# Kernel tuning notes

Hardware: AMD Instinct MI355X
Metric: run time of the kernel (lower is better)

## Reference

```python
import jax, jax.numpy as jnp
import numpy as np

N_NODES = 50000
N_EDGES = 600000
D_IN = 128
HID = 128
N_SAGE = 2          # num_layers - 1
N_GRAPHS = 512
BN_EPS = 1e-5


def setup_inputs() -> dict:
    key = jax.random.key(0)
    ks = jax.random.split(key, 12)
    s = 1.0 / np.sqrt(HID)
    x = jax.random.normal(ks[0], (N_NODES, D_IN), dtype=jnp.float32)
    edge_index = jax.random.randint(ks[1], (2, N_EDGES), 0, N_NODES, dtype=jnp.int32)
    batch = jnp.sort(jax.random.randint(ks[2], (N_NODES,), 0, N_GRAPHS, dtype=jnp.int32))
    # GIN MLP: Linear(D_IN,HID) -> ReLU -> Linear(HID,HID)
    gin_w1 = jax.random.normal(ks[3], (D_IN, HID), dtype=jnp.float32) * s
    gin_b1 = jnp.zeros((HID,), jnp.float32)
    gin_w2 = jax.random.normal(ks[4], (HID, HID), dtype=jnp.float32) * s
    gin_b2 = jnp.zeros((HID,), jnp.float32)
    # SAGEConv layers: lin_l (neighbors, with bias), lin_r (root, no bias)
    sage_wl = jax.random.normal(ks[5], (N_SAGE, HID, HID), dtype=jnp.float32) * s
    sage_bl = jnp.zeros((N_SAGE, HID), jnp.float32)
    sage_wr = jax.random.normal(ks[6], (N_SAGE, HID, HID), dtype=jnp.float32) * s
    # BatchNorm per layer (3 layers)
    bn_gamma = jnp.ones((1 + N_SAGE, HID), jnp.float32)
    bn_beta = jnp.zeros((1 + N_SAGE, HID), jnp.float32)
    return {"x": x, "edge_index": edge_index, "batch": batch,
            "gin_w1": gin_w1, "gin_b1": gin_b1, "gin_w2": gin_w2, "gin_b2": gin_b2,
            "sage_wl": sage_wl, "sage_bl": sage_bl, "sage_wr": sage_wr,
            "bn_gamma": bn_gamma, "bn_beta": bn_beta}


def _batchnorm(h, gamma, beta):
    # training-mode BN over the node dimension (biased variance, as torch)
    mu = jnp.mean(h, axis=0)
    var = jnp.var(h, axis=0)
    return gamma * (h - mu) * jax.lax.rsqrt(var + BN_EPS) + beta


def reference(x, edge_index, batch, gin_w1, gin_b1, gin_w2, gin_b2,
              sage_wl, sage_bl, sage_wr, bn_gamma, bn_beta):
    n = x.shape[0]
    src, dst = edge_index[0], edge_index[1]

    # ---- Layer 0: GINConv (eps=0): mlp(x + sum_{j->i} x_j) ----
    agg = jax.ops.segment_sum(x[src], dst, num_segments=n)  # [N, D_IN]
    h = x + agg
    h = jax.nn.relu(h @ gin_w1 + gin_b1) @ gin_w2 + gin_b2
    h = jax.nn.relu(_batchnorm(h, bn_gamma[0], bn_beta[0]))
    # dropout is identity (eval mode)

    # degree for mean aggregation (shared across SAGE layers)
    deg = jax.ops.segment_sum(jnp.ones((src.shape[0],), h.dtype), dst, num_segments=n)
    inv_deg = (1.0 / jnp.maximum(deg, 1.0))[:, None]  # [N,1]

    # ---- SAGE layers: lin_l(mean_{j->i} h_j) + lin_r(h_i) ----
    for l in range(N_SAGE):
        neigh = jax.ops.segment_sum(h[src], dst, num_segments=n) * inv_deg
        h = neigh @ sage_wl[l] + sage_bl[l] + h @ sage_wr[l]
        h = jax.nn.relu(_batchnorm(h, bn_gamma[l + 1], bn_beta[l + 1]))

    # ---- global mean pool over batch ids ----
    sums = jax.ops.segment_sum(h, batch, num_segments=N_GRAPHS)  # [G, HID]
    counts = jax.ops.segment_sum(jnp.ones((n,), h.dtype), batch, num_segments=N_GRAPHS)
    return sums / jnp.maximum(counts, 1.0)[:, None]
```

## Files before the change

kernel.cpp:

```cpp
#include <hip/hip_runtime.h>

#define N_NODES 50000
#define N_EDGES 600000
#define HID 128
#define N_GRAPHS 512
#define BN_EPS 1e-5f
#define INV_N (1.0f / 50000.0f)
#define NGROUPS 3125
#define FUSED_GRID 1024
#define IDXCAP 2048

typedef __attribute__((ext_vector_type(8))) short bf16x8;
typedef __attribute__((ext_vector_type(4))) float f32x4;

__device__ __forceinline__ unsigned short f2b(float f) {
    unsigned u = __float_as_uint(f);
    return (unsigned short)((u + 0x7FFFu + ((u >> 16) & 1u)) >> 16);
}
__device__ __forceinline__ float b2f(unsigned short h) {
    return __uint_as_float(((unsigned)h) << 16);
}

__device__ __forceinline__ float stats_sum(const float* __restrict__ s, int idx) {
    float v = 0.f;
#pragma unroll
    for (int r = 0; r < 8; r++) v += s[r * 256 + idx];
    return v;
}

#define CONVX_BLOCKS 6250
#define WCONV_BLOCKS 384
#define DEG_BLOCKS   2344
__global__ __launch_bounds__(256) void prep_kernel(
    const float* __restrict__ x, const float* __restrict__ gw1, const float* __restrict__ gw2,
    const float* __restrict__ swl, const float* __restrict__ swr, const int* __restrict__ dst,
    unsigned short* __restrict__ x16, unsigned short* __restrict__ wt, int* __restrict__ deg)
{
    int b = blockIdx.x;
    int t = threadIdx.x;
    if (b < CONVX_BLOCKS) {
        int gid = b * 256 + t;
        int i = gid >> 5, l = gid & 31;
        if (i >= N_NODES) return;
        int c0 = l * 4;
        float4 v = *(const float4*)(x + (size_t)i * 128 + c0);
        ushort4 o;
        o.x = f2b(v.x); o.y = f2b(v.y); o.z = f2b(v.z); o.w = f2b(v.w);
        *(ushort4*)(x16 + (size_t)i * 128 + c0) = o;
    } else if (b < CONVX_BLOCKS + WCONV_BLOCKS) {
        int gid = (b - CONVX_BLOCKS) * 256 + t;
        int m = gid >> 14;
        int e = gid & 16383;
        int k = e >> 7;
        int n = e & 127;
        const float* src = (m == 0) ? gw1 : (m == 1) ? gw2 : (m == 2) ? swl
                         : (m == 3) ? swr : (m == 4) ? (swl + 16384) : (swr + 16384);
        wt[m * 16384 + n * 128 + k] = f2b(src[k * 128 + n]);
    } else {
        int e = (b - CONVX_BLOCKS - WCONV_BLOCKS) * 256 + t;
        if (e < N_EDGES) atomicAdd(&deg[dst[e]], 1);
    }
}

#define ALLOC_BLOCKS 196
__global__ __launch_bounds__(256) void alloc_kernel(int* __restrict__ cursor,
                                                    int* __restrict__ row_beg,
                                                    float* __restrict__ inv_deg,
                                                    int* __restrict__ total,
                                                    const int* __restrict__ batch,
                                                    int* __restrict__ gstart) {
    if (blockIdx.x >= ALLOC_BLOCKS) {
        int g = (blockIdx.x - ALLOC_BLOCKS) * 256 + threadIdx.x;
        if (g > N_GRAPHS) return;
        int lo = 0, hi = N_NODES;
        while (lo < hi) {
            int mid = (lo + hi) >> 1;
            if (batch[mid] < g) lo = mid + 1; else hi = mid;
        }
        gstart[g] = lo;
        return;
    }
    __shared__ int tmp[256];
    __shared__ int base;
    int i = blockIdx.x * 256 + threadIdx.x;
    int d = (i < N_NODES) ? cursor[i] : 0;
    tmp[threadIdx.x] = d;
    __syncthreads();
#pragma unroll
    for (int off = 1; off < 256; off <<= 1) {
        int v = (threadIdx.x >= off) ? tmp[threadIdx.x - off] : 0;
        __syncthreads();
        tmp[threadIdx.x] += v;
        __syncthreads();
    }
    if (threadIdx.x == 255) base = atomicAdd(total, tmp[255]);
    __syncthreads();
    if (i < N_NODES) {
        int b = base + tmp[threadIdx.x] - d;
        row_beg[i] = b;
        cursor[i] = b;
        inv_deg[i] = 1.0f / fmaxf((float)d, 1.0f);
    }
}

__global__ void csr_fill_kernel(const int* __restrict__ src, const int* __restrict__ dst,
                                int* __restrict__ cursor, unsigned short* __restrict__ csr_src, int nE) {
    int e = blockIdx.x * blockDim.x + threadIdx.x;
    if (e < nE) {
        int pos = atomicAdd(&cursor[dst[e]], 1);
        csr_src[pos] = (unsigned short)src[e];
    }
}

template<bool AFF>
__device__ __forceinline__ void gather_row(
    const unsigned short* __restrict__ feat,
    const unsigned short* __restrict__ csr_src,
    const unsigned short* __restrict__ idxbuf,
    bool lds_ok, int ebeg, int beg, int deg, int c0,
    const float (&cc)[8], const float (&ss)[8], float (&a)[8])
{
#pragma unroll
    for (int j = 0; j < 8; j++) a[j] = 0.f;
    if (lds_ok) {
        const int off = beg - ebeg;
        int e = 0;
        for (; e + 7 < deg; e += 8) {
            int s[8];
#pragma unroll
            for (int u = 0; u < 8; u++) s[u] = idxbuf[off + e + u];
            bf16x8 v[8];
#pragma unroll
            for (int u = 0; u < 8; u++)
                v[u] = *(const bf16x8*)(feat + (size_t)s[u] * 128 + c0);
#pragma unroll
            for (int u = 0; u < 8; u++)
#pragma unroll
                for (int j = 0; j < 8; j++) {
                    float tv = b2f((unsigned short)v[u][j]);
                    if (AFF) tv = fmaxf(tv * cc[j] + ss[j], 0.f);
                    a[j] += tv;
                }
        }
        for (; e + 3 < deg; e += 4) {
            int s[4];
#pragma unroll
            for (int u = 0; u < 4; u++) s[u] = idxbuf[off + e + u];
            bf16x8 v[4];
#pragma unroll
            for (int u = 0; u < 4; u++)
                v[u] = *(const bf16x8*)(feat + (size_t)s[u] * 128 + c0);
#pragma unroll
            for (int u = 0; u < 4; u++)
#pragma unroll
                for (int j = 0; j < 8; j++) {
                    float tv = b2f((unsigned short)v[u][j]);
                    if (AFF) tv = fmaxf(tv * cc[j] + ss[j], 0.f);
                    a[j] += tv;
                }
        }
        for (; e < deg; e++) {
            int s0 = idxbuf[off + e];
            bf16x8 v0 = *(const bf16x8*)(feat + (size_t)s0 * 128 + c0);
#pragma unroll
            for (int j = 0; j < 8; j++) {
                float tv = b2f((unsigned short)v0[j]);
                if (AFF) tv = fmaxf(tv * cc[j] + ss[j], 0.f);
                a[j] += tv;
            }
        }
    } else {
        for (int e = beg; e < beg + deg; e++) {
            int s0 = csr_src[e];
            bf16x8 v0 = *(const bf16x8*)(feat + (size_t)s0 * 128 + c0);
#pragma unroll
            for (int j = 0; j < 8; j++) {
                float tv = b2f((unsigned short)v0[j]);
                if (AFF) tv = fmaxf(tv * cc[j] + ss[j], 0.f);
                a[j] += tv;
            }
        }
    }
}

__global__ __launch_bounds__(256, 2) void fused_gin_kernel(
    const unsigned short* __restrict__ X,
    const int* __restrict__ row_beg, const int* __restrict__ row_end,
    const unsigned short* __restrict__ csr_src,
    const unsigned short* __restrict__ W1t, const unsigned short* __restrict__ W2t,
    const float* __restrict__ b1, const float* __restrict__ b2,
    float* __restrict__ stats_out, unsigned short* __restrict__ Hout, int ngroups)
{
    __shared__ unsigned short idxbuf[IDXCAP];
    __shared__ unsigned short aT[16][136];
    __shared__ unsigned short t1[16][136];
    __shared__ float red[128];

    const int t = threadIdx.x;
    const int wave = t >> 6;
    const int lane = t & 63;
    const int m16 = lane & 15;
    const int quad = lane >> 4;
    const int k0 = quad * 8;
    const int colbase = wave * 32;
    const int nslot = t >> 4;
    const int c0 = (t & 15) * 8;

    bf16x8 w1f[2][4], w2f[2][4];
#pragma unroll
    for (int ct = 0; ct < 2; ct++) {
        int col = colbase + ct * 16 + m16;
#pragma unroll
        for (int kc = 0; kc < 4; kc++) {
            w1f[ct][kc] = *(const bf16x8*)(W1t + (size_t)col * 128 + kc * 32 + k0);
            w2f[ct][kc] = *(const bf16x8*)(W2t + (size_t)col * 128 + kc * 32 + k0);
        }
    }
    f32x4 bs1[2], bs2[2];
#pragma unroll
    for (int ct = 0; ct < 2; ct++) {
        bs1[ct] = *(const f32x4*)(b1 + colbase + ct * 16 + quad * 4);
        bs2[ct] = *(const f32x4*)(b2 + colbase + ct * 16 + quad * 4);
    }

    float psum[2][4], psq[2][4];
#pragma unroll
    for (int ct = 0; ct < 2; ct++)
#pragma unroll
        for (int r = 0; r < 4; r++) { psum[ct][r] = 0.f; psq[ct][r] = 0.f; }

    float dcc[8], dss[8];
#pragma unroll
    for (int j = 0; j < 8; j++) { dcc[j] = 0.f; dss[j] = 0.f; }

    for (int g = blockIdx.x; g < ngroups; g += gridDim.x) {
        const int node0 = g * 16;
        const int node = node0 + nslot;
        const int ebeg = row_beg[node0];
        const int ecnt = row_end[node0 + 15] - ebeg;
        const bool lds_ok = (ecnt <= IDXCAP);
        if (lds_ok)
            for (int i = t; i < ecnt; i += 256) idxbuf[i] = csr_src[ebeg + i];
        bf16x8 vself = *(const bf16x8*)(X + (size_t)node * 128 + c0);
        const int beg = row_beg[node];
        const int deg = row_end[node] - beg;
        __syncthreads();

        float a[8];
        gather_row<false>(X, csr_src, idxbuf, lds_ok, ebeg, beg, deg, c0, dcc, dss, a);

        bf16x8 arow;
#pragma unroll
        for (int j = 0; j < 8; j++)
            arow[j] = (short)f2b(a[j] + b2f((unsigned short)vself[j]));
        *(bf16x8*)&aT[nslot][c0] = arow;
        __syncthreads();

        bf16x8 af[4];
#pragma unroll
        for (int kc = 0; kc < 4; kc++)
            af[kc] = *(const bf16x8*)&aT[m16][kc * 32 + k0];
        f32x4 acc[2];
        acc[0] = (f32x4){0.f, 0.f, 0.f, 0.f};
        acc[1] = (f32x4){0.f, 0.f, 0.f, 0.f};
#pragma unroll
        for (int kc = 0; kc < 4; kc++)
#pragma unroll
            for (int ct = 0; ct < 2; ct++)
                acc[ct] = __builtin_amdgcn_mfma_f32_16x16x32_bf16(w1f[ct][kc], af[kc], acc[ct], 0, 0, 0);
#pragma unroll
        for (int ct = 0; ct < 2; ct++) {
            f32x4 v = acc[ct] + bs1[ct];
            ushort4 o;
            o.x = f2b(fmaxf(v[0], 0.f));
            o.y = f2b(fmaxf(v[1], 0.f));
            o.z = f2b(fmaxf(v[2], 0.f));
            o.w = f2b(fmaxf(v[3], 0.f));
            *(ushort4*)&t1[m16][colbase + ct * 16 + quad * 4] = o;
        }
        __syncthreads();

        bf16x8 tf[4];
#pragma unroll
        for (int kc = 0; kc < 4; kc++)
            tf[kc] = *(const bf16x8*)&t1[m16][kc * 32 + k0];
        f32x4 acc2[2];
        acc2[0] = (f32x4){0.f, 0.f, 0.f, 0.f};
        acc2[1] = (f32x4){0.f, 0.f, 0.f, 0.f};
#pragma unroll
        for (int kc = 0; kc < 4; kc++)
#pragma unroll
            for (int ct = 0; ct < 2; ct++)
                acc2[ct] = __builtin_amdgcn_mfma_f32_16x16x32_bf16(w2f[ct][kc], tf[kc], acc2[ct], 0, 0, 0);

        const int orow = node0 + m16;
#pragma unroll
        for (int ct = 0; ct < 2; ct++) {
            f32x4 v = acc2[ct] + bs2[ct];
            int col = colbase + ct * 16 + quad * 4;
#pragma unroll
            for (int r = 0; r < 4; r++) { psum[ct][r] += v[r]; psq[ct][r] += v[r] * v[r]; }
            ushort4 o;
            o.x = f2b(v[0]); o.y = f2b(v[1]); o.z = f2b(v[2]); o.w = f2b(v[3]);
            *(ushort4*)(Hout + (size_t)orow * 128 + col) = o;
        }
    }

#pragma unroll
    for (int ct = 0; ct < 2; ct++)
#pragma unroll
        for (int r = 0; r < 4; r++)
#pragma unroll
            for (int mask = 1; mask <= 8; mask <<= 1) {
                psum[ct][r] += __shfl_xor(psum[ct][r], mask, 64);
                psq[ct][r]  += __shfl_xor(psq[ct][r], mask, 64);
            }
    __syncthreads();
    if (m16 == 0)
#pragma unroll
        for (int ct = 0; ct < 2; ct++)
#pragma unroll
            for (int r = 0; r < 4; r++)
                red[colbase + ct * 16 + quad * 4 + r] = psum[ct][r];
    __syncthreads();
    if (t < 128) atomicAdd(&stats_out[(blockIdx.x & 7) * 256 + t], red[t]);
    __syncthreads();
    if (m16 == 0)
#pragma unroll
        for (int ct = 0; ct < 2; ct++)
#pragma unroll
            for (int r = 0; r < 4; r++)
                red[colbase + ct * 16 + quad * 4 + r] = psq[ct][r];
    __syncthreads();
    if (t < 128) atomicAdd(&stats_out[(blockIdx.x & 7) * 256 + 128 + t], red[t]);
}

__global__ __launch_bounds__(256, 2) void fused_sage_kernel(
    const unsigned short* __restrict__ Hin,
    const int* __restrict__ row_beg, const int* __restrict__ row_end,
    const unsigned short* __restrict__ csr_src,
    const float* __restrict__ stats_in, const float* __restrict__ gamma,
    const float* __restrict__ beta, const float* __restrict__ inv_deg,
    const unsigned short* __restrict__ Wlt, const unsigned short* __restrict__ Wrt,
    const float* __restrict__ bias, float* __restrict__ stats_out,
    unsigned short* __restrict__ Hout, int ngroups)
{
    __shared__ unsigned short idxbuf[IDXCAP];
    __shared__ unsigned short aT[16][136];
    __shared__ unsigned short hT[16][136];
    __shared__ float red[128];

    const int t = threadIdx.x;
    const int wave = t >> 6;
    const int lane = t & 63;
    const int m16 = lane & 15;
    const int quad = lane >> 4;
    const int k0 = quad * 8;
    const int colbase = wave * 32;
    const int nslot = t >> 4;
    const int c0 = (t & 15) * 8;

    float cc[8], ss[8];
#pragma unroll
    for (int j = 0; j < 8; j++) {
        int col = c0 + j;
        float mu = stats_sum(stats_in, col) * INV_N;
        float var = stats_sum(stats_in, 128 + col) * INV_N - mu * mu;
        float rs = rsqrtf(var + BN_EPS);
        float c = gamma[col] * rs;
        cc[j] = c;
        ss[j] = beta[col] - mu * c;
    }

    bf16x8 wl[2][4], wr[2][4];
#pragma unroll
    for (int ct = 0; ct < 2; ct++) {
        int col = colbase + ct * 16 + m16;
#pragma unroll
        for (int kc = 0; kc < 4; kc++) {
            wl[ct][kc] = *(const bf16x8*)(Wlt + (size_t)col * 128 + kc * 32 + k0);
            wr[ct][kc] = *(const bf16x8*)(Wrt + (size_t)col * 128 + kc * 32 + k0);
        }
    }
    f32x4 bs[2];
#pragma unroll
    for (int ct = 0; ct < 2; ct++)
        bs[ct] = *(const f32x4*)(bias + colbase + ct * 16 + quad * 4);

    float psum[2][4], psq[2][4];
#pragma unroll
    for (int ct = 0; ct < 2; ct++)
#pragma unroll
        for (int r = 0; r < 4; r++) { psum[ct][r] = 0.f; psq[ct][r] = 0.f; }

    for (int g = blockIdx.x; g < ngroups; g += gridDim.x) {
        const int node0 = g * 16;
        const int node = node0 + nslot;
        const int ebeg = row_beg[node0];
        const int ecnt = row_end[node0 + 15] - ebeg;
        const bool lds_ok = (ecnt <= IDXCAP);
        if (lds_ok)
            for (int i = t; i < ecnt; i += 256) idxbuf[i] = csr_src[ebeg + i];
        bf16x8 vself = *(const bf16x8*)(Hin + (size_t)node * 128 + c0);
        const float sc = inv_deg[node];
        const int beg = row_beg[node];
        const int deg = row_end[node] - beg;
        __syncthreads();

        float a[8];
        gather_row<true>(Hin, csr_src, idxbuf, lds_ok, ebeg, beg, deg, c0, cc, ss, a);

        bf16x8 arow, hrow;
#pragma unroll
        for (int j = 0; j < 8; j++) {
            arow[j] = (short)f2b(a[j] * sc);
            hrow[j] = (short)f2b(fmaxf(b2f((unsigned short)vself[j]) * cc[j] + ss[j], 0.f));
        }
        *(bf16x8*)&aT[nslot][c0] = arow;
        *(bf16x8*)&hT[nslot][c0] = hrow;
        __syncthreads();

        bf16x8 a1[4], a2[4];
#pragma unroll
        for (int kc = 0; kc < 4; kc++) {
            a1[kc] = *(const bf16x8*)&aT[m16][kc * 32 + k0];
            a2[kc] = *(const bf16x8*)&hT[m16][kc * 32 + k0];
        }
        f32x4 acc[2];
        acc[0] = (f32x4){0.f, 0.f, 0.f, 0.f};
        acc[1] = (f32x4){0.f, 0.f, 0.f, 0.f};
#pragma unroll
        for (int kc = 0; kc < 4; kc++)
#pragma unroll
            for (int ct = 0; ct < 2; ct++) {
                acc[ct] = __builtin_amdgcn_mfma_f32_16x16x32_bf16(wl[ct][kc], a1[kc], acc[ct], 0, 0, 0);
                acc[ct] = __builtin_amdgcn_mfma_f32_16x16x32_bf16(wr[ct][kc], a2[kc], acc[ct], 0, 0, 0);
            }

        const int orow = node0 + m16;
#pragma unroll
        for (int ct = 0; ct < 2; ct++) {
            f32x4 v = acc[ct] + bs[ct];
            int col = colbase + ct * 16 + quad * 4;
#pragma unroll
            for (int r = 0; r < 4; r++) { psum[ct][r] += v[r]; psq[ct][r] += v[r] * v[r]; }
            ushort4 o;
            o.x = f2b(v[0]); o.y = f2b(v[1]); o.z = f2b(v[2]); o.w = f2b(v[3]);
            *(ushort4*)(Hout + (size_t)orow * 128 + col) = o;
        }
    }

#pragma unroll
    for (int ct = 0; ct < 2; ct++)
#pragma unroll
        for (int r = 0; r < 4; r++)
#pragma unroll
            for (int mask = 1; mask <= 8; mask <<= 1) {
                psum[ct][r] += __shfl_xor(psum[ct][r], mask, 64);
                psq[ct][r]  += __shfl_xor(psq[ct][r], mask, 64);
            }
    __syncthreads();
    if (m16 == 0)
#pragma unroll
        for (int ct = 0; ct < 2; ct++)
#pragma unroll
            for (int r = 0; r < 4; r++)
                red[colbase + ct * 16 + quad * 4 + r] = psum[ct][r];
    __syncthreads();
    if (t < 128) atomicAdd(&stats_out[(blockIdx.x & 7) * 256 + t], red[t]);
    __syncthreads();
    if (m16 == 0)
#pragma unroll
        for (int ct = 0; ct < 2; ct++)
#pragma unroll
            for (int r = 0; r < 4; r++)
                red[colbase + ct * 16 + quad * 4 + r] = psq[ct][r];
    __syncthreads();
    if (t < 128) atomicAdd(&stats_out[(blockIdx.x & 7) * 256 + 128 + t], red[t]);
}

__global__ __launch_bounds__(128) void pool_mean_kernel(const unsigned short* __restrict__ h,
                                                        const int* __restrict__ gstart,
                                                        const float* __restrict__ stats,
                                                        const float* __restrict__ gamma,
                                                        const float* __restrict__ beta,
                                                        float* __restrict__ out) {
    __shared__ float red[8][128];
    int g = blockIdx.x;
    int t = threadIdx.x;
    int lane = t & 15, grp = t >> 4;
    int c0 = lane * 8;
    float c[8], b[8];
#pragma unroll
    for (int j = 0; j < 8; j++) {
        int col = c0 + j;
        float mu = stats_sum(stats, col) * INV_N;
        float var = stats_sum(stats, 128 + col) * INV_N - mu * mu;
        float rs = rsqrtf(var + BN_EPS);
        c[j] = gamma[col] * rs;
        b[j] = beta[col] - mu * c[j];
    }
    int beg = gstart[g];
    int end = gstart[g + 1];
    float s[8];
#pragma unroll
    for (int j = 0; j < 8; j++) s[j] = 0.f;
    for (int i = beg + grp; i < end; i += 8) {
        bf16x8 v = *(const bf16x8*)(h + (size_t)i * 128 + c0);
#pragma unroll
        for (int j = 0; j < 8; j++)
            s[j] += fmaxf(b2f((unsigned short)v[j]) * c[j] + b[j], 0.f);
    }
#pragma unroll
    for (int j = 0; j < 8; j++) red[grp][c0 + j] = s[j];
    __syncthreads();
    if (t < 16) {
        float cnt = fmaxf((float)(end - beg), 1.0f);
        int cc0 = t * 8;
#pragma unroll
        for (int j = 0; j < 8; j++) {
            float tot = 0.f;
#pragma unroll
            for (int r = 0; r < 8; r++) tot += red[r][cc0 + j];
            out[(size_t)g * 128 + cc0 + j] = tot / cnt;
        }
    }
}

extern "C" void kernel_launch(void* const* d_in, const int* in_sizes, int n_in,
                              void* d_out, int out_size, void* d_ws, size_t ws_size,
                              hipStream_t stream) {
    const float* x    = (const float*)d_in[0];
    const int*   ei   = (const int*)d_in[1];
    const int*   src  = ei;
    const int*   dst  = ei + N_EDGES;
    const int*   batch = (const int*)d_in[2];
    const float* gw1  = (const float*)d_in[3];
    const float* gb1  = (const float*)d_in[4];
    const float* gw2  = (const float*)d_in[5];
    const float* gb2  = (const float*)d_in[6];
    const float* swl  = (const float*)d_in[7];
    const float* sbl  = (const float*)d_in[8];
    const float* swr  = (const float*)d_in[9];
    const float* bng  = (const float*)d_in[10];
    const float* bnb  = (const float*)d_in[11];
    float* out = (float*)d_out;

    float* ws = (float*)d_ws;
    unsigned short* x16    = (unsigned short*)(ws + 0);
    unsigned short* h_a    = (unsigned short*)(ws + 3200000);
    unsigned short* h_b    = (unsigned short*)(ws + 6400000);
    unsigned short* wt     = (unsigned short*)(ws + 12800000);
    float*          inv_deg= ws + 12850000;
    int*            row_beg= (int*)(ws + 12900000);
    int*            cursor = (int*)(ws + 12950000);
    int*            total  = cursor + 50000;
    float*          stats  = (float*)(cursor + 50001);
    unsigned short* csr_src= (unsigned short*)(ws + 13100000);
    int*            gstart = (int*)(ws + 13700000);

    hipMemsetAsync(cursor, 0, (50001 + 3 * 8 * 256) * sizeof(int), stream);

    prep_kernel<<<CONVX_BLOCKS + WCONV_BLOCKS + DEG_BLOCKS, 256, 0, stream>>>(
        x, gw1, gw2, swl, swr, dst, x16, wt, cursor);

    alloc_kernel<<<ALLOC_BLOCKS + 3, 256, 0, stream>>>(cursor, row_beg, inv_deg, total, batch, gstart);
    csr_fill_kernel<<<(N_EDGES + 255) / 256, 256, 0, stream>>>(src, dst, cursor, csr_src, N_EDGES);

    fused_gin_kernel<<<FUSED_GRID, 256, 0, stream>>>(
        x16, row_beg, cursor, csr_src, wt + 0 * 16384, wt + 1 * 16384,
        gb1, gb2, stats + 0 * 2048, h_a, NGROUPS);

    fused_sage_kernel<<<FUSED_GRID, 256, 0, stream>>>(
        h_a, row_beg, cursor, csr_src, stats + 0 * 2048, bng + 0 * HID, bnb + 0 * HID,
        inv_deg, wt + 2 * 16384, wt + 3 * 16384, sbl + 0 * HID, stats + 1 * 2048, h_b, NGROUPS);

    fused_sage_kernel<<<FUSED_GRID, 256, 0, stream>>>(
        h_b, row_beg, cursor, csr_src, stats + 1 * 2048, bng + 1 * HID, bnb + 1 * HID,
        inv_deg, wt + 4 * 16384, wt + 5 * 16384, sbl + 1 * HID, stats + 2 * 2048, h_a, NGROUPS);

    pool_mean_kernel<<<N_GRAPHS, 128, 0, stream>>>(
        h_a, gstart, stats + 2 * 2048, bng + 2 * HID, bnb + 2 * HID, out);
}
```

Before: 313.7 us.

## Split BN+ReLU into separate pass and launch one block per node group

Moves the BatchNorm affine and ReLU out of the SAGE gather loop into a standalone elementwise finish kernel, so neighbor gathers read already-activated features instead of applying the affine to every gathered element. The persistent grid-stride loop is replaced with one block per 16-node group. Weight fragments are loaded per half-tile to cut register pressure, which allows launch bounds of 6 blocks per SM, and the LDS index buffer is halved. This trades an extra read and write of the hidden matrix, plus two extra launches, for cheaper gathers and higher occupancy, and it reloads the weights in every block.

Result: slower. 320.5 us (+2.2%).

```diff
diff --git a/kernel.cpp b/kernel.cpp
--- a/kernel.cpp
+++ b/kernel.cpp
@@ -7,8 +7,7 @@
 #define BN_EPS 1e-5f
 #define INV_N (1.0f / 50000.0f)
 #define NGROUPS 3125
-#define FUSED_GRID 1024
-#define IDXCAP 2048
+#define IDXCAP 1024
 
 typedef __attribute__((ext_vector_type(8))) short bf16x8;
 typedef __attribute__((ext_vector_type(4))) float f32x4;
@@ -112,13 +111,11 @@
     }
 }
 
-template<bool AFF>
-__device__ __forceinline__ void gather_row(
+__device__ __forceinline__ void gather8(
     const unsigned short* __restrict__ feat,
     const unsigned short* __restrict__ csr_src,
     const unsigned short* __restrict__ idxbuf,
-    bool lds_ok, int ebeg, int beg, int deg, int c0,
-    const float (&cc)[8], const float (&ss)[8], float (&a)[8])
+    bool lds_ok, int ebeg, int beg, int deg, int c0, float (&a)[8])
 {
 #pragma unroll
     for (int j = 0; j < 8; j++) a[j] = 0.f;
@@ -136,11 +133,8 @@
 #pragma unroll
             for (int u = 0; u < 8; u++)
 #pragma unroll
-                for (int j = 0; j < 8; j++) {
-                    float tv = b2f((unsigned short)v[u][j]);
-                    if (AFF) tv = fmaxf(tv * cc[j] + ss[j], 0.f);
-                    a[j] += tv;
-                }
+                for (int j = 0; j < 8; j++)
+                    a[j] += b2f((unsigned short)v[u][j]);
         }
         for (; e + 3 < deg; e += 4) {
             int s[4];
@@ -153,43 +147,62 @@
 #pragma unroll
             for (int u = 0; u < 4; u++)
 #pragma unroll
-                for (int j = 0; j < 8; j++) {
-                    float tv = b2f((unsigned short)v[u][j]);
-                    if (AFF) tv = fmaxf(tv * cc[j] + ss[j], 0.f);
-                    a[j] += tv;
-                }
+                for (int j = 0; j < 8; j++)
+                    a[j] += b2f((unsigned short)v[u][j]);
         }
         for (; e < deg; e++) {
             int s0 = idxbuf[off + e];
             bf16x8 v0 = *(const bf16x8*)(feat + (size_t)s0 * 128 + c0);
 #pragma unroll
-            for (int j = 0; j < 8; j++) {
-                float tv = b2f((unsigned short)v0[j]);
-                if (AFF) tv = fmaxf(tv * cc[j] + ss[j], 0.f);
-                a[j] += tv;
-            }
+            for (int j = 0; j < 8; j++)
+                a[j] += b2f((unsigned short)v0[j]);
         }
     } else {
         for (int e = beg; e < beg + deg; e++) {
             int s0 = csr_src[e];
             bf16x8 v0 = *(const bf16x8*)(feat + (size_t)s0 * 128 + c0);
 #pragma unroll
-            for (int j = 0; j < 8; j++) {
-                float tv = b2f((unsigned short)v0[j]);
-                if (AFF) tv = fmaxf(tv * cc[j] + ss[j], 0.f);
-                a[j] += tv;
-            }
-        }
-    }
-}
-
-__global__ __launch_bounds__(256, 2) void fused_gin_kernel(
+            for (int j = 0; j < 8; j++)
+                a[j] += b2f((unsigned short)v0[j]);
+        }
+    }
+}
+
+__global__ __launch_bounds__(256) void finish_kernel(
+    const unsigned short* __restrict__ Hpre, const float* __restrict__ stats,
+    const float* __restrict__ gamma, const float* __restrict__ beta,
+    unsigned short* __restrict__ Hact)
+{
+    __shared__ float cs[2][128];
+    int t = threadIdx.x;
+    if (t < 128) {
+        float mu = stats_sum(stats, t) * INV_N;
+        float var = stats_sum(stats, 128 + t) * INV_N - mu * mu;
+        float rs = rsqrtf(var + BN_EPS);
+        float c = gamma[t] * rs;
+        cs[0][t] = c;
+        cs[1][t] = beta[t] - mu * c;
+    }
+    __syncthreads();
+    int gid = blockIdx.x * 256 + t;
+    int node = gid >> 4, l = gid & 15;
+    if (node >= N_NODES) return;
+    int c0 = l * 8;
+    bf16x8 v = *(const bf16x8*)(Hpre + (size_t)node * 128 + c0);
+    bf16x8 o;
+#pragma unroll
+    for (int j = 0; j < 8; j++)
+        o[j] = (short)f2b(fmaxf(b2f((unsigned short)v[j]) * cs[0][c0 + j] + cs[1][c0 + j], 0.f));
+    *(bf16x8*)(Hact + (size_t)node * 128 + c0) = o;
+}
+
+__global__ __launch_bounds__(256, 6) void fused_gin_kernel(
     const unsigned short* __restrict__ X,
     const int* __restrict__ row_beg, const int* __restrict__ row_end,
     const unsigned short* __restrict__ csr_src,
     const unsigned short* __restrict__ W1t, const unsigned short* __restrict__ W2t,
     const float* __restrict__ b1, const float* __restrict__ b2,
-    float* __restrict__ stats_out, unsigned short* __restrict__ Hout, int ngroups)
+    float* __restrict__ stats_out, unsigned short* __restrict__ Hout)
 {
     __shared__ unsigned short idxbuf[IDXCAP];
     __shared__ unsigned short aT[16][136];
@@ -202,148 +215,115 @@
     const int m16 = lane & 15;
     const int quad = lane >> 4;
     const int k0 = quad * 8;
-    const int colbase = wave * 32;
     const int nslot = t >> 4;
     const int c0 = (t & 15) * 8;
 
-    bf16x8 w1f[2][4], w2f[2][4];
-#pragma unroll
-    for (int ct = 0; ct < 2; ct++) {
-        int col = colbase + ct * 16 + m16;
+    const int g = blockIdx.x;
+    const int node0 = g * 16;
+    const int node = node0 + nslot;
+    const int ebeg = row_beg[node0];
+    const int ecnt = row_end[node0 + 15] - ebeg;
+    const bool lds_ok = (ecnt <= IDXCAP);
+    if (lds_ok)
+        for (int i = t; i < ecnt; i += 256) idxbuf[i] = csr_src[ebeg + i];
+    bf16x8 vself = *(const bf16x8*)(X + (size_t)node * 128 + c0);
+    const int beg = row_beg[node];
+    const int deg = row_end[node] - beg;
+    __syncthreads();
+
+    float a[8];
+    gather8(X, csr_src, idxbuf, lds_ok, ebeg, beg, deg, c0, a);
+
+    bf16x8 arow;
+#pragma unroll
+    for (int j = 0; j < 8; j++)
+        arow[j] = (short)f2b(a[j] + b2f((unsigned short)vself[j]));
+    *(bf16x8*)&aT[nslot][c0] = arow;
+    __syncthreads();
+
+#pragma unroll
+    for (int p = 0; p < 2; p++) {
+        const int cb = p * 64 + wave * 16;
+        bf16x8 wf[4];
+#pragma unroll
+        for (int kc = 0; kc < 4; kc++)
+            wf[kc] = *(const bf16x8*)(W1t + (size_t)(cb + m16) * 128 + kc * 32 + k0);
+        f32x4 bsv = *(const f32x4*)(b1 + cb + quad * 4);
+        f32x4 acc = (f32x4){0.f, 0.f, 0.f, 0.f};
 #pragma unroll
         for (int kc = 0; kc < 4; kc++) {
-            w1f[ct][kc] = *(const bf16x8*)(W1t + (size_t)col * 128 + kc * 32 + k0);
-            w2f[ct][kc] = *(const bf16x8*)(W2t + (size_t)col * 128 + kc * 32 + k0);
-        }
-    }
-    f32x4 bs1[2], bs2[2];
-#pragma unroll
-    for (int ct = 0; ct < 2; ct++) {
-        bs1[ct] = *(const f32x4*)(b1 + colbase + ct * 16 + quad * 4);
-        bs2[ct] = *(const f32x4*)(b2 + colbase + ct * 16 + quad * 4);
-    }
+            bf16x8 af = *(const bf16x8*)&aT[m16][kc * 32 + k0];
+            acc = __builtin_amdgcn_mfma_f32_16x16x32_bf16(wf[kc], af, acc, 0, 0, 0);
+        }
+        f32x4 v = acc + bsv;
+        ushort4 o;
+        o.x = f2b(fmaxf(v[0], 0.f));
+        o.y = f2b(fmaxf(v[1], 0.f));
+        o.z = f2b(fmaxf(v[2], 0.f));
+        o.w = f2b(fmaxf(v[3], 0.f));
+        *(ushort4*)&t1[m16][cb + quad * 4] = o;
+    }
+    __syncthreads();
 
     float psum[2][4], psq[2][4];
 #pragma unroll
-    for (int ct = 0; ct < 2; ct++)
-#pragma unroll
-        for (int r = 0; r < 4; r++) { psum[ct][r] = 0.f; psq[ct][r] = 0.f; }
-
-    float dcc[8], dss[8];
-#pragma unroll
-    for (int j = 0; j < 8; j++) { dcc[j] = 0.f; dss[j] = 0.f; }
-
-    for (int g = blockIdx.x; g < ngroups; g += gridDim.x) {
-        const int node0 = g * 16;
-        const int node = node0 + nslot;
-        const int ebeg = row_beg[node0];
-        const int ecnt = row_end[node0 + 15] - ebeg;
-        const bool lds_ok = (ecnt <= IDXCAP);
-        if (lds_ok)
-            for (int i = t; i < ecnt; i += 256) idxbuf[i] = csr_src[ebeg + i];
-        bf16x8 vself = *(const bf16x8*)(X + (size_t)node * 128 + c0);
-        const int beg = row_beg[node];
-        const int deg = row_end[node] - beg;
-        __syncthreads();
-
-        float a[8];
-        gather_row<false>(X, csr_src, idxbuf, lds_ok, ebeg, beg, deg, c0, dcc, dss, a);
-
-        bf16x8 arow;
-#pragma unroll
-        for (int j = 0; j < 8; j++)
-            arow[j] = (short)f2b(a[j] + b2f((unsigned short)vself[j]));
-        *(bf16x8*)&aT[nslot][c0] = arow;
-        __syncthreads();
-
-        bf16x8 af[4];
+    for (int p = 0; p < 2; p++) {
+        const int cb = p * 64 + wave * 16;
+        bf16x8 wf[4];
 #pragma unroll
         for (int kc = 0; kc < 4; kc++)
-            af[kc] = *(const bf16x8*)&aT[m16][kc * 32 + k0];
-        f32x4 acc[2];
-        acc[0] = (f32x4){0.f, 0.f, 0.f, 0.f};
-        acc[1] = (f32x4){0.f, 0.f, 0.f, 0.f};
-#pragma unroll
-        for (int kc = 0; kc < 4; kc++)
-#pragma unroll
-            for (int ct = 0; ct < 2; ct++)
-                acc[ct] = __builtin_amdgcn_mfma_f32_16x16x32_bf16(w1f[ct][kc], af[kc], acc[ct], 0, 0, 0);
-#pragma unroll
-        for (int ct = 0; ct < 2; ct++) {
-            f32x4 v = acc[ct] + bs1[ct];
-            ushort4 o;
-            o.x = f2b(fmaxf(v[0], 0.f));
-            o.y = f2b(fmaxf(v[1], 0.f));
-            o.z = f2b(fmaxf(v[2], 0.f));
-            o.w = f2b(fmaxf(v[3], 0.f));
-            *(ushort4*)&t1[m16][colbase + ct * 16 + quad * 4] = o;
-        }
-        __syncthreads();
-
-        bf16x8 tf[4];
-#pragma unroll
-        for (int kc = 0; kc < 4; kc++)
-            tf[kc] = *(const bf16x8*)&t1[m16][kc * 32 + k0];
-        f32x4 acc2[2];
-        acc2[0] = (f32x4){0.f, 0.f, 0.f, 0.f};
-        acc2[1] = (f32x4){0.f, 0.f, 0.f, 0.f};
-#pragma unroll
-        for (int kc = 0; kc < 4; kc++)
-#pragma unroll
-            for (int ct = 0; ct < 2; ct++)
-                acc2[ct] = __builtin_amdgcn_mfma_f32_16x16x32_bf16(w2f[ct][kc], tf[kc], acc2[ct], 0, 0, 0);
-
-        const int orow = node0 + m16;
-#pragma unroll
-        for (int ct = 0; ct < 2; ct++) {
-            f32x4 v = acc2[ct] + bs2[ct];
-            int col = colbase + ct * 16 + quad * 4;
-#pragma unroll
-            for (int r = 0; r < 4; r++) { psum[ct][r] += v[r]; psq[ct][r] += v[r] * v[r]; }
-            ushort4 o;
-            o.x = f2b(v[0]); o.y = f2b(v[1]); o.z = f2b(v[2]); o.w = f2b(v[3]);
-            *(ushort4*)(Hout + (size_t)orow * 128 + col) = o;
-        }
-    }
-
-#pragma unroll
-    for (int ct = 0; ct < 2; ct++)
+            wf[kc] = *(const bf16x8*)(W2t + (size_t)(cb + m16) * 128 + kc * 32 + k0);
+        f32x4 bsv = *(const f32x4*)(b2 + cb + quad * 4);
+        f32x4 acc = (f32x4){0.f, 0.f, 0.f, 0.f};
+#pragma unroll
+        for (int kc = 0; kc < 4; kc++) {
+            bf16x8 tf = *(const bf16x8*)&t1[m16][kc * 32 + k0];
+            acc = __builtin_amdgcn_mfma_f32_16x16x32_bf16(wf[kc], tf, acc, 0, 0, 0);
+        }
+        f32x4 v = acc + bsv;
+#pragma unroll
+        for (int r = 0; r < 4; r++) { psum[p][r] = v[r]; psq[p][r] = v[r] * v[r]; }
+        ushort4 o;
+        o.x = f2b(v[0]); o.y = f2b(v[1]); o.z = f2b(v[2]); o.w = f2b(v[3]);
+        *(ushort4*)(Hout + (size_t)(node0 + m16) * 128 + cb + quad * 4) = o;
+    }
+
+#pragma unroll
+    for (int p = 0; p < 2; p++)
 #pragma unroll
         for (int r = 0; r < 4; r++)
 #pragma unroll
             for (int mask = 1; mask <= 8; mask <<= 1) {
-                psum[ct][r] += __shfl_xor(psum[ct][r], mask, 64);
-                psq[ct][r]  += __shfl_xor(psq[ct][r], mask, 64);
+                psum[p][r] += __shfl_xor(psum[p][r], mask, 64);
+                psq[p][r]  += __shfl_xor(psq[p][r], mask, 64);
             }
-    __syncthreads();
     if (m16 == 0)
 #pragma unroll
-        for (int ct = 0; ct < 2; ct++)
+        for (int p = 0; p < 2; p++)
 #pragma unroll
             for (int r = 0; r < 4; r++)
-                red[colbase + ct * 16 + quad * 4 + r] = psum[ct][r];
-    __syncthreads();
-    if (t < 128) atomicAdd(&stats_out[(blockIdx.x & 7) * 256 + t], red[t]);
+                red[p * 64 + wave * 16 + quad * 4 + r] = psum[p][r];
+    __syncthreads();
+    if (t < 128) atomicAdd(&stats_out[(g & 7) * 256 + t], red[t]);
     __syncthreads();
     if (m16 == 0)
 #pragma unroll
-        for (int ct = 0; ct < 2; ct++)
+        for (int p = 0; p < 2; p++)
 #pragma unroll
             for (int r = 0; r < 4; r++)
-                red[colbase + ct * 16 + quad * 4 + r] = psq[ct][r];
-    __syncthreads();
-    if (t < 128) atomicAdd(&stats_out[(blockIdx.x & 7) * 256 + 128 + t], red[t]);
-}
-
-__global__ __launch_bounds__(256, 2) void fused_sage_kernel(
+                red[p * 64 + wave * 16 + quad * 4 + r] = psq[p][r];
+    __syncthreads();
+    if (t < 128) atomicAdd(&stats_out[(g & 7) * 256 + 128 + t], red[t]);
+}
+
+__global__ __launch_bounds__(256, 6) void fused_sage_kernel(
     const unsigned short* __restrict__ Hin,
     const int* __restrict__ row_beg, const int* __restrict__ row_end,
     const unsigned short* __restrict__ csr_src,
-    const float* __restrict__ stats_in, const float* __restrict__ gamma,
-    const float* __restrict__ beta, const float* __restrict__ inv_deg,
+    const float* __restrict__ inv_deg,
     const unsigned short* __restrict__ Wlt, const unsigned short* __restrict__ Wrt,
     const float* __restrict__ bias, float* __restrict__ stats_out,
-    unsigned short* __restrict__ Hout, int ngroups)
+    unsigned short* __restrict__ Hout)
 {
     __shared__ unsigned short idxbuf[IDXCAP];
     __shared__ unsigned short aT[16][136];
@@ -356,127 +336,87 @@
     const int m16 = lane & 15;
     const int quad = lane >> 4;
     const int k0 = quad * 8;
-    const int colbase = wave * 32;
     const int nslot = t >> 4;
     const int c0 = (t & 15) * 8;
 
-    float cc[8], ss[8];
-#pragma unroll
-    for (int j = 0; j < 8; j++) {
-        int col = c0 + j;
-        float mu = stats_sum(stats_in, col) * INV_N;
-        float var = stats_sum(stats_in, 128 + col) * INV_N - mu * mu;
-        float rs = rsqrtf(var + BN_EPS);
-        float c = gamma[col] * rs;
-        cc[j] = c;
-        ss[j] = beta[col] - mu * c;
-    }
-
-    bf16x8 wl[2][4], wr[2][4];
-#pragma unroll
-    for (int ct = 0; ct < 2; ct++) {
-        int col = colbase + ct * 16 + m16;
+    const int g = blockIdx.x;
+    const int node0 = g * 16;
+    const int node = node0 + nslot;
+    const int ebeg = row_beg[node0];
+    const int ecnt = row_end[node0 + 15] - ebeg;
+    const bool lds_ok = (ecnt <= IDXCAP);
+    if (lds_ok)
+        for (int i = t; i < ecnt; i += 256) idxbuf[i] = csr_src[ebeg + i];
+    bf16x8 vself = *(const bf16x8*)(Hin + (size_t)node * 128 + c0);
+    const float sc = inv_deg[node];
+    const int beg = row_beg[node];
+    const int deg = row_end[node] - beg;
+    __syncthreads();
+
+    float a[8];
+    gather8(Hin, csr_src, idxbuf, lds_ok, ebeg, beg, deg, c0, a);
+
+    bf16x8 arow;
+#pragma unroll
+    for (int j = 0; j < 8; j++)
+        arow[j] = (short)f2b(a[j] * sc);
+    *(bf16x8*)&aT[nslot][c0] = arow;
+    *(bf16x8*)&hT[nslot][c0] = vself;
+    __syncthreads();
+
+    float psum[2][4], psq[2][4];
+#pragma unroll
+    for (int p = 0; p < 2; p++) {
+        const int cb = p * 64 + wave * 16;
+        bf16x8 wl[4], wr[4];
 #pragma unroll
         for (int kc = 0; kc < 4; kc++) {
-            wl[ct][kc] = *(const bf16x8*)(Wlt + (size_t)col * 128 + kc * 32 + k0);
-            wr[ct][kc] = *(const bf16x8*)(Wrt + (size_t)col * 128 + kc * 32 + k0);
-        }
-    }
-    f32x4 bs[2];
-#pragma unroll
-    for (int ct = 0; ct < 2; ct++)
-        bs[ct] = *(const f32x4*)(bias + colbase + ct * 16 + quad * 4);
-
-    float psum[2][4], psq[2][4];
-#pragma unroll
-    for (int ct = 0; ct < 2; ct++)
-#pragma unroll
-        for (int r = 0; r < 4; r++) { psum[ct][r] = 0.f; psq[ct][r] = 0.f; }
-
-    for (int g = blockIdx.x; g < ngroups; g += gridDim.x) {
-        const int node0 = g * 16;
-        const int node = node0 + nslot;
-        const int ebeg = row_beg[node0];
-        const int ecnt = row_end[node0 + 15] - ebeg;
-        const bool lds_ok = (ecnt <= IDXCAP);
-        if (lds_ok)
-            for (int i = t; i < ecnt; i += 256) idxbuf[i] = csr_src[ebeg + i];
-        bf16x8 vself = *(const bf16x8*)(Hin + (size_t)node * 128 + c0);
-        const float sc = inv_deg[node];
-        const int beg = row_beg[node];
-        const int deg = row_end[node] - beg;
-        __syncthreads();
-
-        float a[8];
-        gather_row<true>(Hin, csr_src, idxbuf, lds_ok, ebeg, beg, deg, c0, cc, ss, a);
-
-        bf16x8 arow, hrow;
-#pragma unroll
-        for (int j = 0; j < 8; j++) {
-            arow[j] = (short)f2b(a[j] * sc);
-            hrow[j] = (short)f2b(fmaxf(b2f((unsigned short)vself[j]) * cc[j] + ss[j], 0.f));
-        }
-        *(bf16x8*)&aT[nslot][c0] = arow;
-        *(bf16x8*)&hT[nslot][c0] = hrow;
-        __syncthreads();
-
-        bf16x8 a1[4], a2[4];
+            wl[kc] = *(const bf16x8*)(Wlt + (size_t)(cb + m16) * 128 + kc * 32 + k0);
+            wr[kc] = *(const bf16x8*)(Wrt + (size_t)(cb + m16) * 128 + kc * 32 + k0);
+        }
+        f32x4 bsv = *(const f32x4*)(bias + cb + quad * 4);
+        f32x4 acc = (f32x4){0.f, 0.f, 0.f, 0.f};
 #pragma unroll
         for (int kc = 0; kc < 4; kc++) {
-            a1[kc] = *(const bf16x8*)&aT[m16][kc * 32 + k0];
-            a2[kc] = *(const bf16x8*)&hT[m16][kc * 32 + k0];
-        }
-        f32x4 acc[2];
-        acc[0] = (f32x4){0.f, 0.f, 0.f, 0.f};
-        acc[1] = (f32x4){0.f, 0.f, 0.f, 0.f};
-#pragma unroll
-        for (int kc = 0; kc < 4; kc++)
-#pragma unroll
-            for (int ct = 0; ct < 2; ct++) {
-                acc[ct] = __builtin_amdgcn_mfma_f32_16x16x32_bf16(wl[ct][kc], a1[kc], acc[ct], 0, 0, 0);
-                acc[ct] = __builtin_amdgcn_mfma_f32_16x16x32_bf16(wr[ct][kc], a2[kc], acc[ct], 0, 0, 0);
+            bf16x8 a1 = *(const bf16x8*)&aT[m16][kc * 32 + k0];
+            bf16x8 a2 = *(const bf16x8*)&hT[m16][kc * 32 + k0];
+            acc = __builtin_amdgcn_mfma_f32_16x16x32_bf16(wl[kc], a1, acc, 0, 0, 0);
+            acc = __builtin_amdgcn_mfma_f32_16x16x32_bf16(wr[kc], a2, acc, 0, 0, 0);
+        }
+        f32x4 v = acc + bsv;
+#pragma unroll
+        for (int r = 0; r < 4; r++) { psum[p][r] = v[r]; psq[p][r] = v[r] * v[r]; }
+        ushort4 o;
+        o.x = f2b(v[0]); o.y = f2b(v[1]); o.z = f2b(v[2]); o.w = f2b(v[3]);
+        *(ushort4*)(Hout + (size_t)(node0 + m16) * 128 + cb + quad * 4) = o;
+    }
+
+#pragma unroll
+    for (int p = 0; p < 2; p++)
+#pragma unroll
+        for (int r = 0; r < 4; r++)
+#pragma unroll
+            for (int mask = 1; mask <= 8; mask <<= 1) {
+                psum[p][r] += __shfl_xor(psum[p][r], mask, 64);
+                psq[p][r]  += __shfl_xor(psq[p][r], mask, 64);
             }
-
-        const int orow = node0 + m16;
-#pragma unroll
-        for (int ct = 0; ct < 2; ct++) {
-            f32x4 v = acc[ct] + bs[ct];
-            int col = colbase + ct * 16 + quad * 4;
-#pragma unroll
-            for (int r = 0; r < 4; r++) { psum[ct][r] += v[r]; psq[ct][r] += v[r] * v[r]; }
-            ushort4 o;
-            o.x = f2b(v[0]); o.y = f2b(v[1]); o.z = f2b(v[2]); o.w = f2b(v[3]);
-            *(ushort4*)(Hout + (size_t)orow * 128 + col) = o;
-        }
-    }
-
-#pragma unroll
-    for (int ct = 0; ct < 2; ct++)
-#pragma unroll
-        for (int r = 0; r < 4; r++)
-#pragma unroll
-            for (int mask = 1; mask <= 8; mask <<= 1) {
-                psum[ct][r] += __shfl_xor(psum[ct][r], mask, 64);
-                psq[ct][r]  += __shfl_xor(psq[ct][r], mask, 64);
-            }
-    __syncthreads();
     if (m16 == 0)
 #pragma unroll
-        for (int ct = 0; ct < 2; ct++)
+        for (int p = 0; p < 2; p++)
 #pragma unroll
             for (int r = 0; r < 4; r++)
-                red[colbase + ct * 16 + quad * 4 + r] = psum[ct][r];
-    __syncthreads();
-    if (t < 128) atomicAdd(&stats_out[(blockIdx.x & 7) * 256 + t], red[t]);
+                red[p * 64 + wave * 16 + quad * 4 + r] = psum[p][r];
+    __syncthreads();
+    if (t < 128) atomicAdd(&stats_out[(g & 7) * 256 + t], red[t]);
     __syncthreads();
     if (m16 == 0)
 #pragma unroll
-        for (int ct = 0; ct < 2; ct++)
+        for (int p = 0; p < 2; p++)
 #pragma unroll
             for (int r = 0; r < 4; r++)
-                red[colbase + ct * 16 + quad * 4 + r] = psq[ct][r];
-    __syncthreads();
-    if (t < 128) atomicAdd(&stats_out[(blockIdx.x & 7) * 256 + 128 + t], red[t]);
+                red[p * 64 + wave * 16 + quad * 4 + r] = psq[p][r];
+    __syncthreads();
+    if (t < 128) atomicAdd(&stats_out[(g & 7) * 256 + 128 + t], red[t]);
 }
 
 __global__ __launch_bounds__(128) void pool_mean_kernel(const unsigned short* __restrict__ h,
@@ -548,8 +488,8 @@
 
     float* ws = (float*)d_ws;
     unsigned short* x16    = (unsigned short*)(ws + 0);
-    unsigned short* h_a    = (unsigned short*)(ws + 3200000);
-    unsigned short* h_b    = (unsigned short*)(ws + 6400000);
+    unsigned short* h_p    = (unsigned short*)(ws + 3200000);
+    unsigned short* h_act  = (unsigned short*)(ws + 6400000);
     unsigned short* wt     = (unsigned short*)(ws + 12800000);
     float*          inv_deg= ws + 12850000;
     int*            row_beg= (int*)(ws + 12900000);
@@ -567,18 +507,24 @@
     alloc_kernel<<<ALLOC_BLOCKS + 3, 256, 0, stream>>>(cursor, row_beg, inv_deg, total, batch, gstart);
     csr_fill_kernel<<<(N_EDGES + 255) / 256, 256, 0, stream>>>(src, dst, cursor, csr_src, N_EDGES);
 
-    fused_gin_kernel<<<FUSED_GRID, 256, 0, stream>>>(
+    fused_gin_kernel<<<NGROUPS, 256, 0, stream>>>(
         x16, row_beg, cursor, csr_src, wt + 0 * 16384, wt + 1 * 16384,
-        gb1, gb2, stats + 0 * 2048, h_a, NGROUPS);
-
-    fused_sage_kernel<<<FUSED_GRID, 256, 0, stream>>>(
-        h_a, row_beg, cursor, csr_src, stats + 0 * 2048, bng + 0 * HID, bnb + 0 * HID,
-        inv_deg, wt + 2 * 16384, wt + 3 * 16384, sbl + 0 * HID, stats + 1 * 2048, h_b, NGROUPS);
-
-    fused_sage_kernel<<<FUSED_GRID, 256, 0, stream>>>(
-        h_b, row_beg, cursor, csr_src, stats + 1 * 2048, bng + 1 * HID, bnb + 1 * HID,
-        inv_deg, wt + 4 * 16384, wt + 5 * 16384, sbl + 1 * HID, stats + 2 * 2048, h_a, NGROUPS);
+        gb1, gb2, stats + 0 * 2048, h_p);
+
+    finish_kernel<<<NGROUPS, 256, 0, stream>>>(
+        h_p, stats + 0 * 2048, bng + 0 * HID, bnb + 0 * HID, h_act);
+
+    fused_sage_kernel<<<NGROUPS, 256, 0, stream>>>(
+        h_act, row_beg, cursor, csr_src, inv_deg,
+        wt + 2 * 16384, wt + 3 * 16384, sbl + 0 * HID, stats + 1 * 2048, h_p);
+
+    finish_kernel<<<NGROUPS, 256, 0, stream>>>(
+        h_p, stats + 1 * 2048, bng + 1 * HID, bnb + 1 * HID, h_act);
+
+    fused_sage_kernel<<<NGROUPS, 256, 0, stream>>>(
+        h_act, row_beg, cursor, csr_src, inv_deg,
+        wt + 4 * 16384, wt + 5 * 16384, sbl + 1 * HID, stats + 2 * 2048, h_p);
 
     pool_mean_kernel<<<N_GRAPHS, 128, 0, stream>>>(
-        h_a, gstart, stats + 2 * 2048, bng + 2 * HID, bnb + 2 * HID, out);
-}
+        h_p, gstart, stats + 2 * 2048, bng + 2 * HID, bnb + 2 * HID, out);
+}
```
